# Kernel optimization log

Hardware: AMD Instinct MI355X
Metric: run time of the kernel (lower is better)

## Reference

```python
import jax, jax.numpy as jnp
import numpy as np

EPS = 1e-12

def _spectral_normalize(W, u):
    # torch spectral_norm (eval-time math): v = normalize(W^T u), sigma = u^T W v
    u = jax.lax.stop_gradient(u)
    v = W.T @ u
    v = jax.lax.stop_gradient(v / (jnp.linalg.norm(v) + EPS))
    sigma = u @ (W @ v)
    return W / sigma

def _conv1x1(x, W):
    # 1x1 conv, no bias: (out,in) x (B,in,H,W) -> (B,out,H,W)
    return jnp.einsum('oc,bchw->bohw', W, x)

def setup_inputs() -> dict:
    key = jax.random.key(0)
    ks = jax.random.split(key, 10)
    B, C, H, W = 4, 512, 64, 64
    Cp = C // 8
    return {
        'x': jax.random.normal(ks[0], (B, C, H, W), jnp.float32),
        'Wf': jax.random.normal(ks[1], (Cp, C), jnp.float32) * 0.05,
        'Wg': jax.random.normal(ks[2], (Cp, C), jnp.float32) * 0.05,
        'Wh': jax.random.normal(ks[3], (Cp, C), jnp.float32) * 0.05,
        'Wv': jax.random.normal(ks[4], (C, Cp), jnp.float32) * 0.05,
        'uf': jax.random.normal(ks[5], (Cp,), jnp.float32),
        'ug': jax.random.normal(ks[6], (Cp,), jnp.float32),
        'uh': jax.random.normal(ks[7], (Cp,), jnp.float32),
        'uv': jax.random.normal(ks[8], (C,), jnp.float32),
        'gamma': jax.random.normal(ks[9], (1,), jnp.float32) * 0.1,
    }

def reference(x, Wf, Wg, Wh, Wv, uf, ug, uh, uv, gamma):
    B, C, H, W = x.shape
    Cp = Wf.shape[0]
    N = H * W
    Wf_sn = _spectral_normalize(Wf, uf)
    Wg_sn = _spectral_normalize(Wg, ug)
    Wh_sn = _spectral_normalize(Wh, uh)
    Wv_sn = _spectral_normalize(Wv, uv)
    fx = _conv1x1(x, Wf_sn).reshape(B, Cp, N)   # (B,Cp,N)
    gx = _conv1x1(x, Wg_sn).reshape(B, Cp, N)   # (B,Cp,N)
    # fx^T gx: (B,N,N), unscaled single-head attention, softmax over last dim
    scores = jnp.einsum('bcn,bcm->bnm', fx, gx)
    attn = jax.nn.softmax(scores, axis=-1)
    hx = _conv1x1(x, Wh_sn).reshape(B, Cp, N)
    # hx @ attn: out[b,c,j] = sum_i hx[b,c,i] * attn[b,i,j]
    out = jnp.einsum('bci,bij->bcj', hx, attn).reshape(B, Cp, H, W)
    unscaled = _conv1x1(out, Wv_sn)
    return gamma * unscaled + x
```

## Files before the change

kernel.cpp:

```cpp
#include <hip/hip_runtime.h>


#define NB 4
#define CC 512
#define CP 64
#define NN 4096
#define L2E 1.4426950408889634f

typedef __attribute__((ext_vector_type(8))) short short8;
typedef __attribute__((ext_vector_type(4))) float floatx4;
typedef __attribute__((ext_vector_type(16))) float floatx16;

#define MFMA32(A, B, C) __builtin_amdgcn_mfma_f32_32x32x16_bf16((A), (B), (C), 0, 0, 0)

__device__ __forceinline__ float bf2f_u(unsigned short h) {
    return __uint_as_float((unsigned)h << 16);
}
__device__ __forceinline__ float bf16lo(unsigned v) { return __uint_as_float(v << 16); }
__device__ __forceinline__ float bf16hi(unsigned v) { return __uint_as_float(v & 0xffff0000u); }
__device__ __forceinline__ unsigned short f2bf(float f) {
    unsigned u = __float_as_uint(f);
    u += 0x7fffu + ((u >> 16) & 1u);
    return (unsigned short)(u >> 16);
}
__device__ __forceinline__ unsigned pack2bf(float a, float b) {
    return (unsigned)f2bf(a) | ((unsigned)f2bf(b) << 16);
}
__device__ __forceinline__ float ldS(const void* p, long i, int f32) {
    return f32 ? ((const float*)p)[i] : bf2f_u(((const unsigned short*)p)[i]);
}
__device__ __forceinline__ float4 ld4(const void* p, long i, int f32) {
    if (f32) return *reinterpret_cast<const float4*>((const float*)p + i);
    uint2 v = *reinterpret_cast<const uint2*>((const unsigned short*)p + i);
    return make_float4(bf16lo(v.x), bf16hi(v.x), bf16lo(v.y), bf16hi(v.y));
}
__device__ __forceinline__ short8 as_s8(uint4 v) { return *reinterpret_cast<short8*>(&v); }
__device__ __forceinline__ floatx16 zero16() {
    floatx16 z;
    #pragma unroll
    for (int i = 0; i < 16; ++i) z[i] = 0.f;
    return z;
}
__device__ __forceinline__ unsigned cvtpk_bf16(float a, float b) {
    unsigned r;
    asm("v_cvt_pk_bf16_f32 %0, %1, %2" : "=v"(r) : "v"(a), "v"(b));
    return r;
}
__device__ __forceinline__ void pl32swap(unsigned &a, unsigned &b) {
    asm("v_permlane32_swap_b32 %0, %1" : "+v"(a), "+v"(b));
}
__device__ __forceinline__ float rcpf(float x) {
    float r;
    asm("v_rcp_f32 %0, %1" : "=v"(r) : "v"(x));
    return r;
}
__device__ __forceinline__ float exp2a(float x) {
    float r;
    asm("v_exp_f32 %0, %1" : "=v"(r) : "v"(x));
    return r;
}

__global__ __launch_bounds__(256) void detect_kernel(
    const unsigned* __restrict__ x, int* __restrict__ flag)
{
    __shared__ int red[256];
    const int t = threadIdx.x;
    int bad = 0;
    for (int i = t; i < 4096; i += 256) {
        unsigned w = x[i];
        float f0 = __uint_as_float(w << 16);
        float f1 = __uint_as_float(w & 0xffff0000u);
        float a0 = fabsf(f0), a1 = fabsf(f1);
        if (!(a0 <= 1e3f) || (f0 != 0.f && a0 < 1e-20f)) bad++;
        if (!(a1 <= 1e3f) || (f1 != 0.f && a1 < 1e-20f)) bad++;
    }
    red[t] = bad;
    __syncthreads();
    for (int s = 128; s > 0; s >>= 1) { if (t < s) red[t] += red[t + s]; __syncthreads(); }
    if (t == 0) *flag = (red[0] > 64) ? 1 : 0;
}

__global__ __launch_bounds__(256) void xpose_kernel(
    const void* __restrict__ x, const int* __restrict__ dflag,
    unsigned short* __restrict__ xTF)
{
    const int f32 = *dflag;
    const int nt = blockIdx.x;
    const int b  = blockIdx.y;
    const int n0 = nt * 32;
    const int t = threadIdx.x;
    __shared__ unsigned short xl[32][72];

    const int n_l = t & 31, cg8 = ((t >> 5) & 7) * 8;
    const int q = t >> 6, lo = t & 63;

    for (int slab = 0; slab < 8; ++slab) {
        const int cs = slab * 64;
        float v[8];
        #pragma unroll
        for (int j = 0; j < 8; ++j)
            v[j] = ldS(x, ((long)b * CC + cs + cg8 + j) * NN + n0 + n_l, f32);
        if (slab) __syncthreads();
        unsigned* row = reinterpret_cast<unsigned*>(&xl[n_l][cg8]);
        row[0] = pack2bf(v[0], v[1]);
        row[1] = pack2bf(v[2], v[3]);
        row[2] = pack2bf(v[4], v[5]);
        row[3] = pack2bf(v[6], v[7]);
        __syncthreads();
        const int cb = q * 16 + ((lo >> 5) << 3);
        uint4 val = *reinterpret_cast<const uint4*>(&xl[lo & 31][cb]);
        size_t off = (((size_t)(b * 128 + nt) * 32) + slab * 4 + q) * 512 + (size_t)lo * 8;
        *reinterpret_cast<uint4*>(xTF + off) = val;
    }
}

__global__ __launch_bounds__(512) void sigma_kernel(
    const void* __restrict__ Wf, const void* __restrict__ Wg,
    const void* __restrict__ Wh, const void* __restrict__ Wv,
    const void* __restrict__ uf, const void* __restrict__ ug,
    const void* __restrict__ uh, const void* __restrict__ uv,
    const int* __restrict__ dflag, float* __restrict__ sig)
{
    const int f32 = *dflag;
    const int w = blockIdx.x;
    const void* W;
    const void* u;
    if (w == 0)      { W = Wf; u = uf; }
    else if (w == 1) { W = Wg; u = ug; }
    else if (w == 2) { W = Wh; u = uh; }
    else             { W = Wv; u = uv; }

    __shared__ float us[512];
    __shared__ float red[512];
    const int t = threadIdx.x;
    float S;

    if (w < 3) {
        if (t < 64) us[t] = ldS(u, t, f32);
        __syncthreads();
        float a = 0.f;
        #pragma unroll
        for (int i = 0; i < 64; ++i)
            a = fmaf(ldS(W, (long)i * 512 + t, f32), us[i], a);
        red[t] = a * a;
        __syncthreads();
        #pragma unroll
        for (int s = 256; s > 0; s >>= 1) {
            if (t < s) red[t] += red[t + s];
            __syncthreads();
        }
        S = red[0];
    } else {
        us[t] = ldS(u, t, f32);
        __syncthreads();
        const int g = t >> 6, c = t & 63;
        float a = 0.f;
        #pragma unroll
        for (int k = 0; k < 64; ++k) {
            int i = g + k * 8;
            a = fmaf(ldS(W, (long)i * 64 + c, f32), us[i], a);
        }
        red[t] = a;
        __syncthreads();
        #pragma unroll
        for (int s = 256; s >= 64; s >>= 1) {
            if (t < s) red[t] += red[t + s];
            __syncthreads();
        }
        float ac = (t < 64) ? red[t] : 0.f;
        __syncthreads();
        red[t] = ac * ac;
        __syncthreads();
        #pragma unroll
        for (int s = 256; s > 0; s >>= 1) {
            if (t < s) red[t] += red[t + s];
            __syncthreads();
        }
        S = red[0];
    }
    if (t == 0) sig[w] = (sqrtf(S) + 1e-12f) / S;
}

__global__ __launch_bounds__(256) void wprep_kernel(
    const void* __restrict__ Wf, const void* __restrict__ Wg,
    const void* __restrict__ Wh, const void* __restrict__ Wv,
    const int* __restrict__ dflag, const float* __restrict__ sig,
    unsigned short* __restrict__ WF, unsigned short* __restrict__ WvF)
{
    const int f32 = *dflag;
    const int idx = blockIdx.x * 256 + threadIdx.x;
    if (idx < 12288) {
        const int l   = idx & 63;
        const int kc  = (idx >> 6) & 31;
        const int cpt = (idx >> 11) & 1;
        const int wi  = idx >> 12;
        const void* W = (wi == 0) ? Wf : ((wi == 1) ? Wg : Wh);
        const float sc = sig[wi] * (wi == 0 ? L2E : 1.f);
        const int cp = cpt * 32 + (l & 31);
        const int c  = kc * 16 + ((l >> 5) << 3);
        const long base = (long)cp * CC + c;
        float a0 = ldS(W, base + 0, f32) * sc, a1 = ldS(W, base + 1, f32) * sc;
        float a2 = ldS(W, base + 2, f32) * sc, a3 = ldS(W, base + 3, f32) * sc;
        float a4 = ldS(W, base + 4, f32) * sc, a5 = ldS(W, base + 5, f32) * sc;
        float a6 = ldS(W, base + 6, f32) * sc, a7 = ldS(W, base + 7, f32) * sc;
        uint4 o;
        o.x = pack2bf(a0, a1); o.y = pack2bf(a2, a3);
        o.z = pack2bf(a4, a5); o.w = pack2bf(a6, a7);
        *reinterpret_cast<uint4*>(WF + (size_t)idx * 8) = o;
    } else {
        const int idx2 = idx - 12288;
        const int l   = idx2 & 63;
        const int ks  = (idx2 >> 6) & 1;
        const int cot = idx2 >> 7;
        const float sc = sig[3];
        const int co = cot * 16 + (l & 15);
        const int cp = ks * 32 + ((l >> 4) << 3);
        const long base = (long)co * CP + cp;
        float a0 = ldS(Wv, base + 0, f32) * sc, a1 = ldS(Wv, base + 1, f32) * sc;
        float a2 = ldS(Wv, base + 2, f32) * sc, a3 = ldS(Wv, base + 3, f32) * sc;
        float a4 = ldS(Wv, base + 4, f32) * sc, a5 = ldS(Wv, base + 5, f32) * sc;
        float a6 = ldS(Wv, base + 6, f32) * sc, a7 = ldS(Wv, base + 7, f32) * sc;
        uint4 o;
        o.x = pack2bf(a0, a1); o.y = pack2bf(a2, a3);
        o.z = pack2bf(a4, a5); o.w = pack2bf(a6, a7);
        *reinterpret_cast<uint4*>(WvF + (size_t)idx2 * 8) = o;
    }
}

__global__ __launch_bounds__(256, 4) void proj_kernel(
    const unsigned short* __restrict__ xTF,
    const unsigned short* __restrict__ WF,
    unsigned short* __restrict__ fxF, unsigned short* __restrict__ gxF,
    unsigned short* __restrict__ hxF)
{
    const int t = threadIdx.x;
    const int w = t >> 6, l = t & 63;
    const int b  = blockIdx.y;
    const int zc = blockIdx.z;
    const int wi = zc >> 1, cpt = zc & 1;
    const int nt = blockIdx.x * 4 + w;

    const unsigned short* xb = xTF + ((size_t)(b * 128 + nt) * 32) * 512 + (size_t)l * 8;
    const unsigned short* wb = WF + ((size_t)zc * 32) * 512 + (size_t)l * 8;

    floatx16 accE = zero16(), accO = zero16();
    uint4 x0 = *reinterpret_cast<const uint4*>(xb);
    uint4 w0 = *reinterpret_cast<const uint4*>(wb);
    uint4 x1, w1;

    if (wi == 2) {
        for (int kc = 0; kc < 32; kc += 2) {
            x1 = *reinterpret_cast<const uint4*>(xb + (kc + 1) * 512);
            w1 = *reinterpret_cast<const uint4*>(wb + (kc + 1) * 512);
            accE = MFMA32(as_s8(x0), as_s8(w0), accE);
            if (kc + 2 < 32) {
                x0 = *reinterpret_cast<const uint4*>(xb + (kc + 2) * 512);
                w0 = *reinterpret_cast<const uint4*>(wb + (kc + 2) * 512);
            }
            accO = MFMA32(as_s8(x1), as_s8(w1), accO);
        }
    } else {
        for (int kc = 0; kc < 32; kc += 2) {
            x1 = *reinterpret_cast<const uint4*>(xb + (kc + 1) * 512);
            w1 = *reinterpret_cast<const uint4*>(wb + (kc + 1) * 512);
            accE = MFMA32(as_s8(w0), as_s8(x0), accE);
            if (kc + 2 < 32) {
                x0 = *reinterpret_cast<const uint4*>(xb + (kc + 2) * 512);
                w0 = *reinterpret_cast<const uint4*>(wb + (kc + 2) * 512);
            }
            accO = MFMA32(as_s8(w1), as_s8(x1), accO);
        }
    }

    float a[16];
    #pragma unroll
    for (int i = 0; i < 16; ++i) a[i] = accE[i] + accO[i];

    if (wi < 2) {
        unsigned short* __restrict__ dstF = (wi == 0) ? fxF : gxF;
        #pragma unroll
        for (int kcl = 0; kcl < 2; ++kcl) {
            const int r8 = kcl * 8;
            unsigned u0 = cvtpk_bf16(a[r8 + 0], a[r8 + 1]);
            unsigned u1 = cvtpk_bf16(a[r8 + 2], a[r8 + 3]);
            unsigned u2 = cvtpk_bf16(a[r8 + 4], a[r8 + 5]);
            unsigned u3 = cvtpk_bf16(a[r8 + 6], a[r8 + 7]);
            pl32swap(u0, u2);
            pl32swap(u1, u3);
            uint4 o = make_uint4(u0, u1, u2, u3);
            size_t off = (((size_t)(b * 128 + nt) * 4) + cpt * 2 + kcl) * 512 + (size_t)l * 8;
            *reinterpret_cast<uint4*>(dstF + off) = o;
        }
    } else {
        #pragma unroll
        for (int ich = 0; ich < 2; ++ich) {
            const int r8 = ich * 8;
            unsigned u0 = cvtpk_bf16(a[r8 + 0], a[r8 + 1]);
            unsigned u1 = cvtpk_bf16(a[r8 + 2], a[r8 + 3]);
            unsigned u2 = cvtpk_bf16(a[r8 + 4], a[r8 + 5]);
            unsigned u3 = cvtpk_bf16(a[r8 + 6], a[r8 + 7]);
            pl32swap(u0, u2);
            pl32swap(u1, u3);
            uint4 o = make_uint4(u0, u1, u2, u3);
            size_t off = ((((size_t)(b * 128 + nt) * 2 + ich) * 2) + cpt) * 512 + (size_t)l * 8;
            *reinterpret_cast<uint4*>(hxF + off) = o;
        }
    }
}

__global__ __launch_bounds__(256, 4) void rowstats_kernel(
    const unsigned short* __restrict__ fxF, const unsigned short* __restrict__ gxF,
    float* __restrict__ rl)
{
    const int t = threadIdx.x;
    const int w = t >> 6, l = t & 63, l31 = l & 31, hi = l >> 5;
    const int b = blockIdx.z;
    const int i0 = blockIdx.x * 128 + w * 32;
    const int jbase = blockIdx.y * (NN / 8);

    const unsigned short* fA = fxF + ((size_t)(b * 128 + (i0 >> 5))) * 2048 + (size_t)l * 8;
    uint4 af[4];
    #pragma unroll
    for (int kc = 0; kc < 4; ++kc)
        af[kc] = *reinterpret_cast<const uint4*>(fA + kc * 512);

    const unsigned short* gB = gxF + ((size_t)(b * 128 + (jbase >> 5))) * 2048 + (size_t)l * 8;

    float suml[16];
    #pragma unroll
    for (int r = 0; r < 16; ++r) suml[r] = 0.f;

    uint4 bf0[4], bf1[4];
    auto loadB = [&](uint4* bf, int jt) {
        const unsigned short* p = gB + (size_t)jt * 2048;
        #pragma unroll
        for (int kc = 0; kc < 4; ++kc)
            bf[kc] = *reinterpret_cast<const uint4*>(p + kc * 512);
    };
    auto bodyR = [&](uint4* bf) {
        floatx16 s = zero16();
        #pragma unroll
        for (int kc = 0; kc < 4; ++kc)
            s = MFMA32(as_s8(af[kc]), as_s8(bf[kc]), s);
        #pragma unroll
        for (int r = 0; r < 16; ++r) suml[r] += exp2a(s[r]);
    };

    loadB(bf0, 0);
    for (int jt = 0; jt < 16; jt += 2) {
        loadB(bf1, jt + 1);
        bodyR(bf0);
        if (jt + 2 < 16) loadB(bf0, jt + 2);
        bodyR(bf1);
    }

    #pragma unroll
    for (int r = 0; r < 16; ++r) {
        float v = suml[r];
        v += __shfl_xor(v, 1);
        v += __shfl_xor(v, 2);
        v += __shfl_xor(v, 4);
        v += __shfl_xor(v, 8);
        v += __shfl_xor(v, 16);
        suml[r] = v;
    }
    if (l31 == 0) {
        #pragma unroll
        for (int r = 0; r < 16; ++r) {
            int row = (r & 3) + 8 * (r >> 2) + 4 * hi;
            atomicAdd(&rl[(size_t)b * NN + i0 + row], suml[r]);
        }
    }
}

__global__ __launch_bounds__(256) void scalehx_kernel(
    const float* __restrict__ rl, unsigned short* __restrict__ hxF)
{
    const int idx = blockIdx.x * 256 + threadIdx.x;
    const int l = idx & 63;
    const int r = idx >> 6;
    const int ich = (r >> 1) & 1;
    const int tile = (r >> 2) & 127;
    const int b = r >> 9;
    const int i0 = tile * 32 + ich * 16 + (l >> 5) * 8;
    const float* rp = rl + (size_t)b * NN + i0;
    float4 ra = *reinterpret_cast<const float4*>(rp);
    float4 rb = *reinterpret_cast<const float4*>(rp + 4);
    uint4 v = *reinterpret_cast<uint4*>(hxF + (size_t)idx * 8);
    uint4 ov;
    ov.x = pack2bf(bf16lo(v.x) * rcpf(ra.x), bf16hi(v.x) * rcpf(ra.y));
    ov.y = pack2bf(bf16lo(v.y) * rcpf(ra.z), bf16hi(v.y) * rcpf(ra.w));
    ov.z = pack2bf(bf16lo(v.z) * rcpf(rb.x), bf16hi(v.z) * rcpf(rb.y));
    ov.w = pack2bf(bf16lo(v.w) * rcpf(rb.z), bf16hi(v.w) * rcpf(rb.w));
    *reinterpret_cast<uint4*>(hxF + (size_t)idx * 8) = ov;
}

__global__ __launch_bounds__(256, 4) void pv_kernel(
    const unsigned short* __restrict__ fxF, const unsigned short* __restrict__ gxF,
    const unsigned short* __restrict__ hxF,
    float* __restrict__ opF0, float* __restrict__ opF1,
    float* __restrict__ opF2, float* __restrict__ opF3)
{
    const int t = threadIdx.x;
    const int w = t >> 6, l = t & 63, l31 = l & 31, hi = l >> 5;
    const int igrp = w >> 1, jgrp = w & 1;
    const int b = blockIdx.z;
    const int j0 = blockIdx.x * 64;
    const int isb = blockIdx.y;
    const int tbase = isb * 32 + igrp * 16;

    __shared__ float red[64 * 64];

    uint4 qf[4];
    {
        const unsigned short* gq =
            gxF + ((size_t)(b * 128 + (j0 >> 5) + jgrp)) * 2048 + (size_t)l * 8;
        #pragma unroll
        for (int kc = 0; kc < 4; ++kc)
            qf[kc] = *reinterpret_cast<const uint4*>(gq + kc * 512);
    }

    floatx16 acc0 = zero16(), acc1 = zero16();

    const unsigned short* fb = fxF + ((size_t)(b * 128 + tbase)) * 2048 + (size_t)l * 8;
    const unsigned short* vb = hxF + ((size_t)(b * 128 + tbase)) * 2048 + (size_t)l * 8;

    #pragma unroll 2
    for (int it = 0; it < 16; ++it) {
        const unsigned short* fp = fb + (size_t)it * 2048;
        const unsigned short* vp = vb + (size_t)it * 2048;
        uint4 af[4], vf[4];
        #pragma unroll
        for (int kc = 0; kc < 4; ++kc)
            af[kc] = *reinterpret_cast<const uint4*>(fp + kc * 512);
        vf[0] = *reinterpret_cast<const uint4*>(vp);
        vf[1] = *reinterpret_cast<const uint4*>(vp + 1024);
        vf[2] = *reinterpret_cast<const uint4*>(vp + 512);
        vf[3] = *reinterpret_cast<const uint4*>(vp + 1536);

        floatx16 s = zero16();
        #pragma unroll
        for (int kc = 0; kc < 4; ++kc)
            s = MFMA32(as_s8(af[kc]), as_s8(qf[kc]), s);

        float e[16];
        #pragma unroll
        for (int r = 0; r < 16; ++r) e[r] = exp2a(s[r]);

        unsigned u0 = cvtpk_bf16(e[0], e[1]);
        unsigned u1 = cvtpk_bf16(e[2], e[3]);
        unsigned u2 = cvtpk_bf16(e[4], e[5]);
        unsigned u3 = cvtpk_bf16(e[6], e[7]);
        pl32swap(u0, u2);
        pl32swap(u1, u3);
        uint4 pa0 = make_uint4(u0, u1, u2, u3);
        unsigned u4 = cvtpk_bf16(e[8], e[9]);
        unsigned u5 = cvtpk_bf16(e[10], e[11]);
        unsigned u6 = cvtpk_bf16(e[12], e[13]);
        unsigned u7 = cvtpk_bf16(e[14], e[15]);
        pl32swap(u4, u6);
        pl32swap(u5, u7);
        uint4 pa1 = make_uint4(u4, u5, u6, u7);

        acc0 = MFMA32(as_s8(pa0), as_s8(vf[0]), acc0);
        acc0 = MFMA32(as_s8(pa1), as_s8(vf[1]), acc0);
        acc1 = MFMA32(as_s8(pa0), as_s8(vf[2]), acc1);
        acc1 = MFMA32(as_s8(pa1), as_s8(vf[3]), acc1);
    }

    #pragma unroll
    for (int q = 0; q < 4; ++q)
        *reinterpret_cast<float4*>(&red[(q * 256 + t) * 4]) =
            make_float4(0.f, 0.f, 0.f, 0.f);
    __syncthreads();
    #pragma unroll
    for (int r = 0; r < 16; ++r) {
        int row = jgrp * 32 + (r & 3) + 8 * (r >> 2) + 4 * hi;
        atomicAdd(&red[row * 64 + l31],      acc0[r]);
        atomicAdd(&red[row * 64 + 32 + l31], acc1[r]);
    }
    __syncthreads();

    float* __restrict__ dst = (isb == 0) ? opF0 : ((isb == 1) ? opF1 : ((isb == 2) ? opF2 : opF3));
    #pragma unroll
    for (int q = 0; q < 4; ++q) {
        int idx = q * 256 + t;
        int e2  = idx & 1;
        int ll  = (idx >> 1) & 63;
        int ks  = (idx >> 7) & 1;
        int ntl = idx >> 8;
        int jloc = ntl * 16 + (ll & 15);
        int cp   = ks * 32 + ((ll >> 4) << 3) + e2 * 4;
        float4 v = *reinterpret_cast<const float4*>(&red[jloc * 64 + cp]);
        size_t off = (((size_t)(b * 256 + (j0 >> 4) + ntl) * 2 + ks) * 64 + ll) * 8 + e2 * 4;
        *reinterpret_cast<float4*>(dst + off) = v;
    }
}

__global__ __launch_bounds__(256, 4) void outproj_kernel(
    const void* __restrict__ x,
    const unsigned short* __restrict__ WvF,
    const void* __restrict__ gamma,
    const int* __restrict__ dflag,
    const float* __restrict__ opF0, const float* __restrict__ opF1,
    const float* __restrict__ opF2, const float* __restrict__ opF3,
    void* __restrict__ y)
{
    const int f32 = *dflag;
    const int n0     = blockIdx.x * 64;
    const int cobase = blockIdx.y * 128;
    const int b      = blockIdx.z;
    const int t = threadIdx.x;
    const int wv = t >> 6, l = t & 63, l15 = l & 15, quad = l >> 4;
    const float scale = ldS(gamma, 0, f32);

    __shared__ float tile[128][68];

    floatx4 acc[4][2];
    #pragma unroll
    for (int ns = 0; ns < 4; ++ns)
        #pragma unroll
        for (int ct = 0; ct < 2; ++ct) acc[ns][ct] = (floatx4){0.f, 0.f, 0.f, 0.f};

    #pragma unroll
    for (int ks = 0; ks < 2; ++ks) {
        short8 a[4];
        #pragma unroll
        for (int ns = 0; ns < 4; ++ns) {
            size_t fo = (((size_t)(b * 256 + (n0 >> 4) + ns) * 2 + ks) * 64 + l) * 8;
            float4 s0 = *reinterpret_cast<const float4*>(opF0 + fo);
            float4 s1 = *reinterpret_cast<const float4*>(opF1 + fo);
            float4 s2 = *reinterpret_cast<const float4*>(opF2 + fo);
            float4 s3 = *reinterpret_cast<const float4*>(opF3 + fo);
            float4 t0 = *reinterpret_cast<const float4*>(opF0 + fo + 4);
            float4 t1 = *reinterpret_cast<const float4*>(opF1 + fo + 4);
            float4 t2 = *reinterpret_cast<const float4*>(opF2 + fo + 4);
            float4 t3 = *reinterpret_cast<const float4*>(opF3 + fo + 4);
            float v0 = s0.x + s1.x + s2.x + s3.x;
            float v1 = s0.y + s1.y + s2.y + s3.y;
            float v2 = s0.z + s1.z + s2.z + s3.z;
            float v3 = s0.w + s1.w + s2.w + s3.w;
            float v4 = t0.x + t1.x + t2.x + t3.x;
            float v5 = t0.y + t1.y + t2.y + t3.y;
            float v6 = t0.z + t1.z + t2.z + t3.z;
            float v7 = t0.w + t1.w + t2.w + t3.w;
            uint4 au;
            au.x = pack2bf(v0, v1); au.y = pack2bf(v2, v3);
            au.z = pack2bf(v4, v5); au.w = pack2bf(v6, v7);
            a[ns] = *reinterpret_cast<short8*>(&au);
        }
        #pragma unroll
        for (int ct = 0; ct < 2; ++ct) {
            const int cot = (cobase >> 4) + wv * 2 + ct;
            uint4 bv = *reinterpret_cast<const uint4*>(
                WvF + (((size_t)cot * 2 + ks) * 64 + l) * 8);
            short8 bfr = as_s8(bv);
            #pragma unroll
            for (int ns = 0; ns < 4; ++ns)
                acc[ns][ct] = __builtin_amdgcn_mfma_f32_16x16x32_bf16(
                    a[ns], bfr, acc[ns][ct], 0, 0, 0);
        }
    }

    #pragma unroll
    for (int ns = 0; ns < 4; ++ns)
        #pragma unroll
        for (int ct = 0; ct < 2; ++ct) {
            const int co_l = 32 * wv + 16 * ct + l15;
            const int n_l  = 16 * ns + quad * 4;
            *reinterpret_cast<float4*>(&tile[co_l][n_l]) =
                make_float4(acc[ns][ct][0], acc[ns][ct][1],
                            acc[ns][ct][2], acc[ns][ct][3]);
        }
    __syncthreads();

    #pragma unroll
    for (int q = 0; q < 8; ++q) {
        const int idx = q * 256 + t;
        const int co_l = idx >> 4;
        const int nch  = idx & 15;
        float4 v = *reinterpret_cast<const float4*>(&tile[co_l][nch * 4]);
        const long base = ((long)b * CC + cobase + co_l) * NN + n0 + nch * 4;
        float4 xv = ld4(x, base, f32);
        float o0 = fmaf(scale, v.x, xv.x);
        float o1 = fmaf(scale, v.y, xv.y);
        float o2 = fmaf(scale, v.z, xv.z);
        float o3 = fmaf(scale, v.w, xv.w);
        if (f32) {
            *reinterpret_cast<float4*>((float*)y + base) = make_float4(o0, o1, o2, o3);
        } else {
            uint2 o;
            o.x = pack2bf(o0, o1);
            o.y = pack2bf(o2, o3);
            *reinterpret_cast<uint2*>((unsigned short*)y + base) = o;
        }
    }
}

extern "C" void kernel_launch(void* const* d_in, const int* in_sizes, int n_in,
                              void* d_out, int out_size, void* d_ws, size_t ws_size,
                              hipStream_t stream)
{
    const void* x  = d_in[0];
    const void* Wf = d_in[1];
    const void* Wg = d_in[2];
    const void* Wh = d_in[3];
    const void* Wv = d_in[4];
    const void* uf = d_in[5];
    const void* ug = d_in[6];
    const void* uh = d_in[7];
    const void* uv = d_in[8];
    const void* gm = d_in[9];

    char* base = (char*)d_ws;
    int*   dfl = (int*)(base);
    float* sig = (float*)(base + 512);
    float* rl  = (float*)(base + 1024);
    float* opF0 = (float*)(base + 1024 + 65536);
    float* opF1 = opF0 + (size_t)NB * NN * CP;
    float* opF2 = opF1 + (size_t)NB * NN * CP;
    float* opF3 = opF2 + (size_t)NB * NN * CP;
    unsigned short* fxF = (unsigned short*)(opF3 + (size_t)NB * NN * CP);
    unsigned short* gxF = fxF + (size_t)NB * CP * NN;
    unsigned short* hxF = gxF + (size_t)NB * CP * NN;
    unsigned short* xTF = hxF + (size_t)NB * CP * NN;
    unsigned short* WF  = xTF + (size_t)NB * CC * NN;
    unsigned short* WvF = WF + (size_t)6 * 32 * 64 * 8;

    hipMemsetAsync(rl, 0, (size_t)NB * NN * sizeof(float), stream);

    hipLaunchKernelGGL(detect_kernel, dim3(1), dim3(256), 0, stream,
                       (const unsigned*)x, dfl);
    hipLaunchKernelGGL(xpose_kernel, dim3(128, NB), dim3(256), 0, stream,
                       x, dfl, xTF);
    hipLaunchKernelGGL(sigma_kernel, dim3(4), dim3(512), 0, stream,
                       Wf, Wg, Wh, Wv, uf, ug, uh, uv, dfl, sig);
    hipLaunchKernelGGL(wprep_kernel, dim3(64), dim3(256), 0, stream,
                       Wf, Wg, Wh, Wv, dfl, sig, WF, WvF);
    hipLaunchKernelGGL(proj_kernel, dim3(32, NB, 6), dim3(256), 0, stream,
                       xTF, WF, fxF, gxF, hxF);
    hipLaunchKernelGGL(rowstats_kernel, dim3(NN / 128, 8, NB), dim3(256), 0, stream,
                       fxF, gxF, rl);
    hipLaunchKernelGGL(scalehx_kernel, dim3((NB * CP * NN / 8) / 256), dim3(256), 0, stream,
                       rl, hxF);
    hipLaunchKernelGGL(pv_kernel, dim3(NN / 64, 4, NB), dim3(256), 0, stream,
                       fxF, gxF, hxF, opF0, opF1, opF2, opF3);
    hipLaunchKernelGGL(outproj_kernel, dim3(NN / 64, CC / 128, NB), dim3(256), 0, stream,
                       x, WvF, gm, dfl, opF0, opF1, opF2, opF3, d_out);
}
```

Before: 226.5 us.

## Merge prep kernels into one launch and fold row normalization into pv

The detect, transpose, sigma and weight-prep kernels and the memset of the row-sum buffer are merged into a single prep kernel. Each block recomputes the dtype detection locally, so it no longer has to wait on a separate flag kernel. The scalehx pass, which rescaled hx by the inverse softmax row sums, is removed. Instead, pv_kernel loads the row sums and multiplies the exponentials by their reciprocals before packing to bf16. This removes several launches and a full read/write pass over hx, at the cost of redundant detection reads in every block and extra loads and rcp work inside the pv inner loop.

```diff
diff --git a/kernel.cpp b/kernel.cpp
--- a/kernel.cpp
+++ b/kernel.cpp
@@ -60,170 +60,175 @@
     return r;
 }
 
-__global__ __launch_bounds__(256) void detect_kernel(
-    const unsigned* __restrict__ x, int* __restrict__ flag)
-{
-    __shared__ int red[256];
-    const int t = threadIdx.x;
-    int bad = 0;
-    for (int i = t; i < 4096; i += 256) {
-        unsigned w = x[i];
-        float f0 = __uint_as_float(w << 16);
-        float f1 = __uint_as_float(w & 0xffff0000u);
-        float a0 = fabsf(f0), a1 = fabsf(f1);
-        if (!(a0 <= 1e3f) || (f0 != 0.f && a0 < 1e-20f)) bad++;
-        if (!(a1 <= 1e3f) || (f1 != 0.f && a1 < 1e-20f)) bad++;
-    }
-    red[t] = bad;
-    __syncthreads();
-    for (int s = 128; s > 0; s >>= 1) { if (t < s) red[t] += red[t + s]; __syncthreads(); }
-    if (t == 0) *flag = (red[0] > 64) ? 1 : 0;
-}
-
-__global__ __launch_bounds__(256) void xpose_kernel(
-    const void* __restrict__ x, const int* __restrict__ dflag,
-    unsigned short* __restrict__ xTF)
-{
-    const int f32 = *dflag;
-    const int nt = blockIdx.x;
-    const int b  = blockIdx.y;
-    const int n0 = nt * 32;
-    const int t = threadIdx.x;
-    __shared__ unsigned short xl[32][72];
-
-    const int n_l = t & 31, cg8 = ((t >> 5) & 7) * 8;
-    const int q = t >> 6, lo = t & 63;
-
-    for (int slab = 0; slab < 8; ++slab) {
-        const int cs = slab * 64;
-        float v[8];
-        #pragma unroll
-        for (int j = 0; j < 8; ++j)
-            v[j] = ldS(x, ((long)b * CC + cs + cg8 + j) * NN + n0 + n_l, f32);
-        if (slab) __syncthreads();
-        unsigned* row = reinterpret_cast<unsigned*>(&xl[n_l][cg8]);
-        row[0] = pack2bf(v[0], v[1]);
-        row[1] = pack2bf(v[2], v[3]);
-        row[2] = pack2bf(v[4], v[5]);
-        row[3] = pack2bf(v[6], v[7]);
-        __syncthreads();
-        const int cb = q * 16 + ((lo >> 5) << 3);
-        uint4 val = *reinterpret_cast<const uint4*>(&xl[lo & 31][cb]);
-        size_t off = (((size_t)(b * 128 + nt) * 32) + slab * 4 + q) * 512 + (size_t)lo * 8;
-        *reinterpret_cast<uint4*>(xTF + off) = val;
-    }
-}
-
-__global__ __launch_bounds__(512) void sigma_kernel(
+__global__ __launch_bounds__(256) void prep_kernel(
+    const void* __restrict__ x,
     const void* __restrict__ Wf, const void* __restrict__ Wg,
     const void* __restrict__ Wh, const void* __restrict__ Wv,
     const void* __restrict__ uf, const void* __restrict__ ug,
     const void* __restrict__ uh, const void* __restrict__ uv,
-    const int* __restrict__ dflag, float* __restrict__ sig)
+    unsigned short* __restrict__ xTF, float* __restrict__ rl,
+    float* __restrict__ sig, unsigned short* __restrict__ WF,
+    unsigned short* __restrict__ WvF, int* __restrict__ dfl)
 {
-    const int f32 = *dflag;
-    const int w = blockIdx.x;
-    const void* W;
-    const void* u;
-    if (w == 0)      { W = Wf; u = uf; }
-    else if (w == 1) { W = Wg; u = ug; }
-    else if (w == 2) { W = Wh; u = uh; }
-    else             { W = Wv; u = uv; }
-
-    __shared__ float us[512];
-    __shared__ float red[512];
     const int t = threadIdx.x;
-    float S;
-
-    if (w < 3) {
-        if (t < 64) us[t] = ldS(u, t, f32);
+
+    __shared__ int dred[256];
+    {
+        const unsigned* xw = (const unsigned*)x;
+        int bad = 0;
+        for (int i = t; i < 4096; i += 256) {
+            unsigned w = xw[i];
+            float f0 = __uint_as_float(w << 16);
+            float f1 = __uint_as_float(w & 0xffff0000u);
+            float a0 = fabsf(f0), a1 = fabsf(f1);
+            if (!(a0 <= 1e3f) || (f0 != 0.f && a0 < 1e-20f)) bad++;
+            if (!(a1 <= 1e3f) || (f1 != 0.f && a1 < 1e-20f)) bad++;
+        }
+        dred[t] = bad;
         __syncthreads();
-        float a = 0.f;
-        #pragma unroll
-        for (int i = 0; i < 64; ++i)
-            a = fmaf(ldS(W, (long)i * 512 + t, f32), us[i], a);
-        red[t] = a * a;
-        __syncthreads();
-        #pragma unroll
-        for (int s = 256; s > 0; s >>= 1) {
-            if (t < s) red[t] += red[t + s];
-            __syncthreads();
-        }
-        S = red[0];
+        for (int s = 128; s > 0; s >>= 1) {
+            if (t < s) dred[t] += dred[t + s];
+            __syncthreads();
+        }
+    }
+    const int f32 = (dred[0] > 64) ? 1 : 0;
+    __syncthreads();
+
+    if (blockIdx.x < 4) {
+        const int w = blockIdx.x;
+        if (w == 0 && t == 0) *dfl = f32;
+        const void* W;
+        const void* u;
+        if (w == 0)      { W = Wf; u = uf; }
+        else if (w == 1) { W = Wg; u = ug; }
+        else if (w == 2) { W = Wh; u = uh; }
+        else             { W = Wv; u = uv; }
+
+        __shared__ float us[512];
+        __shared__ float red[512];
+        float S;
+
+        if (w < 3) {
+            if (t < 64) us[t] = ldS(u, t, f32);
+            __syncthreads();
+            float a0 = 0.f, a1 = 0.f;
+            #pragma unroll
+            for (int i = 0; i < 64; ++i) {
+                float uv = us[i];
+                a0 = fmaf(ldS(W, (long)i * 512 + t, f32), uv, a0);
+                a1 = fmaf(ldS(W, (long)i * 512 + t + 256, f32), uv, a1);
+            }
+            red[t] = a0 * a0 + a1 * a1;
+            __syncthreads();
+            #pragma unroll
+            for (int s = 128; s > 0; s >>= 1) {
+                if (t < s) red[t] += red[t + s];
+                __syncthreads();
+            }
+            S = red[0];
+        } else {
+            us[t] = ldS(u, t, f32);
+            us[t + 256] = ldS(u, t + 256, f32);
+            __syncthreads();
+            const int g = t >> 6, c = t & 63;
+            float a = 0.f;
+            #pragma unroll
+            for (int k = 0; k < 128; ++k) {
+                int i = g + (k << 2);
+                a = fmaf(ldS(W, (long)i * 64 + c, f32), us[i], a);
+            }
+            red[t] = a;
+            __syncthreads();
+            if (t < 128) red[t] += red[t + 128];
+            __syncthreads();
+            if (t < 64) red[t] += red[t + 64];
+            __syncthreads();
+            float ac = (t < 64) ? red[t] : 0.f;
+            __syncthreads();
+            red[t] = ac * ac;
+            __syncthreads();
+            #pragma unroll
+            for (int s = 128; s > 0; s >>= 1) {
+                if (t < s) red[t] += red[t + s];
+                __syncthreads();
+            }
+            S = red[0];
+        }
+        const float isig = (sqrtf(S) + 1e-12f) / S;
+        if (t == 0) sig[w] = isig;
+
+        if (w < 3) {
+            const float sc = isig * (w == 0 ? L2E : 1.f);
+            #pragma unroll
+            for (int q = 0; q < 16; ++q) {
+                const int idx = q * 256 + t;
+                const int ll  = idx & 63;
+                const int kc  = (idx >> 6) & 31;
+                const int cpt = (idx >> 11) & 1;
+                const int cp = cpt * 32 + (ll & 31);
+                const int c  = kc * 16 + ((ll >> 5) << 3);
+                const long base = (long)cp * CC + c;
+                float a0 = ldS(W, base + 0, f32) * sc, a1 = ldS(W, base + 1, f32) * sc;
+                float a2 = ldS(W, base + 2, f32) * sc, a3 = ldS(W, base + 3, f32) * sc;
+                float a4 = ldS(W, base + 4, f32) * sc, a5 = ldS(W, base + 5, f32) * sc;
+                float a6 = ldS(W, base + 6, f32) * sc, a7 = ldS(W, base + 7, f32) * sc;
+                uint4 o;
+                o.x = pack2bf(a0, a1); o.y = pack2bf(a2, a3);
+                o.z = pack2bf(a4, a5); o.w = pack2bf(a6, a7);
+                *reinterpret_cast<uint4*>(WF + ((size_t)w * 4096 + idx) * 8) = o;
+            }
+        } else {
+            const float sc = isig;
+            #pragma unroll
+            for (int q = 0; q < 16; ++q) {
+                const int idx = q * 256 + t;
+                const int ll  = idx & 63;
+                const int ks  = (idx >> 6) & 1;
+                const int cot = idx >> 7;
+                const int co = cot * 16 + (ll & 15);
+                const int cp = ks * 32 + ((ll >> 4) << 3);
+                const long base = (long)co * CP + cp;
+                float a0 = ldS(W, base + 0, f32) * sc, a1 = ldS(W, base + 1, f32) * sc;
+                float a2 = ldS(W, base + 2, f32) * sc, a3 = ldS(W, base + 3, f32) * sc;
+                float a4 = ldS(W, base + 4, f32) * sc, a5 = ldS(W, base + 5, f32) * sc;
+                float a6 = ldS(W, base + 6, f32) * sc, a7 = ldS(W, base + 7, f32) * sc;
+                uint4 o;
+                o.x = pack2bf(a0, a1); o.y = pack2bf(a2, a3);
+                o.z = pack2bf(a4, a5); o.w = pack2bf(a6, a7);
+                *reinterpret_cast<uint4*>(WvF + (size_t)idx * 8) = o;
+            }
+        }
     } else {
-        us[t] = ldS(u, t, f32);
-        __syncthreads();
-        const int g = t >> 6, c = t & 63;
-        float a = 0.f;
-        #pragma unroll
-        for (int k = 0; k < 64; ++k) {
-            int i = g + k * 8;
-            a = fmaf(ldS(W, (long)i * 64 + c, f32), us[i], a);
-        }
-        red[t] = a;
-        __syncthreads();
-        #pragma unroll
-        for (int s = 256; s >= 64; s >>= 1) {
-            if (t < s) red[t] += red[t + s];
-            __syncthreads();
-        }
-        float ac = (t < 64) ? red[t] : 0.f;
-        __syncthreads();
-        red[t] = ac * ac;
-        __syncthreads();
-        #pragma unroll
-        for (int s = 256; s > 0; s >>= 1) {
-            if (t < s) red[t] += red[t + s];
-            __syncthreads();
-        }
-        S = red[0];
-    }
-    if (t == 0) sig[w] = (sqrtf(S) + 1e-12f) / S;
-}
-
-__global__ __launch_bounds__(256) void wprep_kernel(
-    const void* __restrict__ Wf, const void* __restrict__ Wg,
-    const void* __restrict__ Wh, const void* __restrict__ Wv,
-    const int* __restrict__ dflag, const float* __restrict__ sig,
-    unsigned short* __restrict__ WF, unsigned short* __restrict__ WvF)
-{
-    const int f32 = *dflag;
-    const int idx = blockIdx.x * 256 + threadIdx.x;
-    if (idx < 12288) {
-        const int l   = idx & 63;
-        const int kc  = (idx >> 6) & 31;
-        const int cpt = (idx >> 11) & 1;
-        const int wi  = idx >> 12;
-        const void* W = (wi == 0) ? Wf : ((wi == 1) ? Wg : Wh);
-        const float sc = sig[wi] * (wi == 0 ? L2E : 1.f);
-        const int cp = cpt * 32 + (l & 31);
-        const int c  = kc * 16 + ((l >> 5) << 3);
-        const long base = (long)cp * CC + c;
-        float a0 = ldS(W, base + 0, f32) * sc, a1 = ldS(W, base + 1, f32) * sc;
-        float a2 = ldS(W, base + 2, f32) * sc, a3 = ldS(W, base + 3, f32) * sc;
-        float a4 = ldS(W, base + 4, f32) * sc, a5 = ldS(W, base + 5, f32) * sc;
-        float a6 = ldS(W, base + 6, f32) * sc, a7 = ldS(W, base + 7, f32) * sc;
-        uint4 o;
-        o.x = pack2bf(a0, a1); o.y = pack2bf(a2, a3);
-        o.z = pack2bf(a4, a5); o.w = pack2bf(a6, a7);
-        *reinterpret_cast<uint4*>(WF + (size_t)idx * 8) = o;
-    } else {
-        const int idx2 = idx - 12288;
-        const int l   = idx2 & 63;
-        const int ks  = (idx2 >> 6) & 1;
-        const int cot = idx2 >> 7;
-        const float sc = sig[3];
-        const int co = cot * 16 + (l & 15);
-        const int cp = ks * 32 + ((l >> 4) << 3);
-        const long base = (long)co * CP + cp;
-        float a0 = ldS(Wv, base + 0, f32) * sc, a1 = ldS(Wv, base + 1, f32) * sc;
-        float a2 = ldS(Wv, base + 2, f32) * sc, a3 = ldS(Wv, base + 3, f32) * sc;
-        float a4 = ldS(Wv, base + 4, f32) * sc, a5 = ldS(Wv, base + 5, f32) * sc;
-        float a6 = ldS(Wv, base + 6, f32) * sc, a7 = ldS(Wv, base + 7, f32) * sc;
-        uint4 o;
-        o.x = pack2bf(a0, a1); o.y = pack2bf(a2, a3);
-        o.z = pack2bf(a4, a5); o.w = pack2bf(a6, a7);
-        *reinterpret_cast<uint4*>(WvF + (size_t)idx2 * 8) = o;
+        const int idx = blockIdx.x - 4;
+        const int nt = idx & 127;
+        const int b  = idx >> 7;
+        const int n0 = nt * 32;
+        __shared__ unsigned short xl[32][72];
+
+        const int gid = idx * 256 + t;
+        if (gid < NB * NN) rl[gid] = 0.f;
+
+        const int n_l = t & 31, cg8 = ((t >> 5) & 7) * 8;
+        const int q = t >> 6, lo = t & 63;
+
+        for (int slab = 0; slab < 8; ++slab) {
+            const int cs = slab * 64;
+            float v[8];
+            #pragma unroll
+            for (int j = 0; j < 8; ++j)
+                v[j] = ldS(x, ((long)b * CC + cs + cg8 + j) * NN + n0 + n_l, f32);
+            __syncthreads();
+            unsigned* row = reinterpret_cast<unsigned*>(&xl[n_l][cg8]);
+            row[0] = pack2bf(v[0], v[1]);
+            row[1] = pack2bf(v[2], v[3]);
+            row[2] = pack2bf(v[4], v[5]);
+            row[3] = pack2bf(v[6], v[7]);
+            __syncthreads();
+            const int cb = q * 16 + ((lo >> 5) << 3);
+            uint4 val = *reinterpret_cast<const uint4*>(&xl[lo & 31][cb]);
+            size_t off = (((size_t)(b * 128 + nt) * 32) + slab * 4 + q) * 512 + (size_t)lo * 8;
+            *reinterpret_cast<uint4*>(xTF + off) = val;
+        }
     }
 }
 
@@ -373,31 +378,9 @@
     }
 }
 
-__global__ __launch_bounds__(256) void scalehx_kernel(
-    const float* __restrict__ rl, unsigned short* __restrict__ hxF)
-{
-    const int idx = blockIdx.x * 256 + threadIdx.x;
-    const int l = idx & 63;
-    const int r = idx >> 6;
-    const int ich = (r >> 1) & 1;
-    const int tile = (r >> 2) & 127;
-    const int b = r >> 9;
-    const int i0 = tile * 32 + ich * 16 + (l >> 5) * 8;
-    const float* rp = rl + (size_t)b * NN + i0;
-    float4 ra = *reinterpret_cast<const float4*>(rp);
-    float4 rb = *reinterpret_cast<const float4*>(rp + 4);
-    uint4 v = *reinterpret_cast<uint4*>(hxF + (size_t)idx * 8);
-    uint4 ov;
-    ov.x = pack2bf(bf16lo(v.x) * rcpf(ra.x), bf16hi(v.x) * rcpf(ra.y));
-    ov.y = pack2bf(bf16lo(v.y) * rcpf(ra.z), bf16hi(v.y) * rcpf(ra.w));
-    ov.z = pack2bf(bf16lo(v.z) * rcpf(rb.x), bf16hi(v.z) * rcpf(rb.y));
-    ov.w = pack2bf(bf16lo(v.w) * rcpf(rb.z), bf16hi(v.w) * rcpf(rb.w));
-    *reinterpret_cast<uint4*>(hxF + (size_t)idx * 8) = ov;
-}
-
 __global__ __launch_bounds__(256, 4) void pv_kernel(
     const unsigned short* __restrict__ fxF, const unsigned short* __restrict__ gxF,
-    const unsigned short* __restrict__ hxF,
+    const unsigned short* __restrict__ hxF, const float* __restrict__ rl,
     float* __restrict__ opF0, float* __restrict__ opF1,
     float* __restrict__ opF2, float* __restrict__ opF3)
 {
@@ -424,6 +407,7 @@
 
     const unsigned short* fb = fxF + ((size_t)(b * 128 + tbase)) * 2048 + (size_t)l * 8;
     const unsigned short* vb = hxF + ((size_t)(b * 128 + tbase)) * 2048 + (size_t)l * 8;
+    const float* rbase = rl + (size_t)b * NN + tbase * 32 + (hi << 2);
 
     #pragma unroll 2
     for (int it = 0; it < 16; ++it) {
@@ -438,6 +422,17 @@
         vf[2] = *reinterpret_cast<const uint4*>(vp + 512);
         vf[3] = *reinterpret_cast<const uint4*>(vp + 1536);
 
+        const float* rp = rbase + it * 32;
+        float4 rv0 = *reinterpret_cast<const float4*>(rp);
+        float4 rv1 = *reinterpret_cast<const float4*>(rp + 8);
+        float4 rv2 = *reinterpret_cast<const float4*>(rp + 16);
+        float4 rv3 = *reinterpret_cast<const float4*>(rp + 24);
+        float ri[16];
+        ri[0] = rcpf(rv0.x); ri[1] = rcpf(rv0.y); ri[2] = rcpf(rv0.z); ri[3] = rcpf(rv0.w);
+        ri[4] = rcpf(rv1.x); ri[5] = rcpf(rv1.y); ri[6] = rcpf(rv1.z); ri[7] = rcpf(rv1.w);
+        ri[8] = rcpf(rv2.x); ri[9] = rcpf(rv2.y); ri[10] = rcpf(rv2.z); ri[11] = rcpf(rv2.w);
+        ri[12] = rcpf(rv3.x); ri[13] = rcpf(rv3.y); ri[14] = rcpf(rv3.z); ri[15] = rcpf(rv3.w);
+
         floatx16 s = zero16();
         #pragma unroll
         for (int kc = 0; kc < 4; ++kc)
@@ -445,7 +440,7 @@
 
         float e[16];
         #pragma unroll
-        for (int r = 0; r < 16; ++r) e[r] = exp2a(s[r]);
+        for (int r = 0; r < 16; ++r) e[r] = exp2a(s[r]) * ri[r];
 
         unsigned u0 = cvtpk_bf16(e[0], e[1]);
         unsigned u1 = cvtpk_bf16(e[2], e[3]);
@@ -627,24 +622,15 @@
     unsigned short* WF  = xTF + (size_t)NB * CC * NN;
     unsigned short* WvF = WF + (size_t)6 * 32 * 64 * 8;
 
-    hipMemsetAsync(rl, 0, (size_t)NB * NN * sizeof(float), stream);
-
-    hipLaunchKernelGGL(detect_kernel, dim3(1), dim3(256), 0, stream,
-                       (const unsigned*)x, dfl);
-    hipLaunchKernelGGL(xpose_kernel, dim3(128, NB), dim3(256), 0, stream,
-                       x, dfl, xTF);
-    hipLaunchKernelGGL(sigma_kernel, dim3(4), dim3(512), 0, stream,
-                       Wf, Wg, Wh, Wv, uf, ug, uh, uv, dfl, sig);
-    hipLaunchKernelGGL(wprep_kernel, dim3(64), dim3(256), 0, stream,
-                       Wf, Wg, Wh, Wv, dfl, sig, WF, WvF);
+    hipLaunchKernelGGL(prep_kernel, dim3(516), dim3(256), 0, stream,
+                       x, Wf, Wg, Wh, Wv, uf, ug, uh, uv,
+                       xTF, rl, sig, WF, WvF, dfl);
     hipLaunchKernelGGL(proj_kernel, dim3(32, NB, 6), dim3(256), 0, stream,
                        xTF, WF, fxF, gxF, hxF);
     hipLaunchKernelGGL(rowstats_kernel, dim3(NN / 128, 8, NB), dim3(256), 0, stream,
                        fxF, gxF, rl);
-    hipLaunchKernelGGL(scalehx_kernel, dim3((NB * CP * NN / 8) / 256), dim3(256), 0, stream,
-                       rl, hxF);
     hipLaunchKernelGGL(pv_kernel, dim3(NN / 64, 4, NB), dim3(256), 0, stream,
-                       fxF, gxF, hxF, opF0, opF1, opF2, opF3);
+                       fxF, gxF, hxF, rl, opF0, opF1, opF2, opF3);
     hipLaunchKernelGGL(outproj_kernel, dim3(NN / 64, CC / 128, NB), dim3(256), 0, stream,
                        x, WvF, gm, dfl, opF0, opF1, opF2, opF3, d_out);
 }
```

New measurement: 236.3 us. +4.3%, slower.
